# Performance work log

Measured on AMD Instinct MI355X. Metric: run time of the kernel, lower is better.

## Reference

```python
import jax, jax.numpy as jnp
import numpy as np

N_NODES = 50000
N_EDGES = 800000
D_IN = 128
D_HID = 128
N_CLASSES = 16
N_GRAPHS = 256


def _gcn_norm(edge_index, num_nodes):
    # PyG GCNConv default: add self-loops, symmetric normalization.
    loops = jnp.arange(num_nodes, dtype=edge_index.dtype)
    src = jnp.concatenate([edge_index[0], loops])
    dst = jnp.concatenate([edge_index[1], loops])
    deg = jax.ops.segment_sum(jnp.ones_like(src, dtype=jnp.float32), dst,
                              num_segments=num_nodes)
    dinv = jnp.where(deg > 0, jax.lax.rsqrt(deg), 0.0)
    norm = dinv[src] * dinv[dst]  # [E + N]
    return src, dst, norm


def _gcn_conv(x, src, dst, norm, W, b, num_nodes):
    h = x @ W                                  # [N, d_out] dense GEMM
    msg = h[src] * norm[:, None]               # gather + scale [E+N, d_out]
    agg = jax.ops.segment_sum(msg, dst, num_segments=num_nodes)
    return agg + b


def setup_inputs() -> dict:
    key = jax.random.key(0)
    ks = jax.random.split(key, 10)
    x = jax.random.normal(ks[0], (N_NODES, D_IN), dtype=jnp.float32)
    edge_index = jax.random.randint(ks[1], (2, N_EDGES), 0, N_NODES, dtype=jnp.int64)
    batch = jnp.sort(jax.random.randint(ks[2], (N_NODES,), 0, N_GRAPHS, dtype=jnp.int64))
    s1 = 1.0 / np.sqrt(D_IN)
    s2 = 1.0 / np.sqrt(D_HID)
    W1 = jax.random.uniform(ks[3], (D_IN, D_HID), jnp.float32, -s1, s1)
    b1 = jnp.zeros((D_HID,), jnp.float32)
    W2 = jax.random.uniform(ks[4], (D_HID, D_HID), jnp.float32, -s2, s2)
    b2 = jnp.zeros((D_HID,), jnp.float32)
    Wc = jax.random.uniform(ks[5], (D_HID, N_CLASSES), jnp.float32, -s2, s2)
    bc = jnp.zeros((N_CLASSES,), jnp.float32)
    return {"x": x, "edge_index": edge_index, "batch": batch,
            "W1": W1, "b1": b1, "W2": W2, "b2": b2, "Wc": Wc, "bc": bc}


def reference(x, edge_index, batch, W1, b1, W2, b2, Wc, bc):
    src, dst, norm = _gcn_norm(edge_index, N_NODES)
    h = _gcn_conv(x, src, dst, norm, W1, b1, N_NODES)
    h = jax.nn.relu(h)  # dropout is identity in eval mode
    h = _gcn_conv(h, src, dst, norm, W2, b2, N_NODES)
    # global mean pool over graph ids
    sums = jax.ops.segment_sum(h, batch, num_segments=N_GRAPHS)
    cnts = jax.ops.segment_sum(jnp.ones((N_NODES,), jnp.float32), batch,
                               num_segments=N_GRAPHS)
    pooled = sums / jnp.maximum(cnts, 1.0)[:, None]  # [G, D_HID]
    return pooled @ Wc + bc  # [G, N_CLASSES]
```

## Files before the change

### kernel.cpp

```cpp
#include <hip/hip_runtime.h>

#define N_NODES 50000
#define N_EDGES 800000
#define D 128
#define N_GRAPHS 256
#define N_CLASSES 16
#define NB_SCAN ((N_NODES + 255) / 256)

typedef unsigned short ushort_t;
typedef unsigned int uint_t;
typedef unsigned char uchar_t;
typedef __attribute__((ext_vector_type(8))) short bf16x8;
typedef __attribute__((ext_vector_type(4))) float f32x4;
typedef __attribute__((ext_vector_type(4))) int i32x4;

__device__ __forceinline__ float bf2f(uint_t u) {
  return __uint_as_float(u << 16);
}
__device__ __forceinline__ uint_t f2bf(float f) {
  uint_t x = __float_as_uint(f);
  return (x + 0x7fffu + ((x >> 16) & 1u)) >> 16;
}
__device__ __forceinline__ void add8(float* acc, uint4 v) {
  acc[0] += bf2f(v.x & 0xffffu);
  acc[1] += bf2f(v.x >> 16);
  acc[2] += bf2f(v.y & 0xffffu);
  acc[3] += bf2f(v.y >> 16);
  acc[4] += bf2f(v.z & 0xffffu);
  acc[5] += bf2f(v.z >> 16);
  acc[6] += bf2f(v.w & 0xffffu);
  acc[7] += bf2f(v.w >> 16);
}

__global__ void k_pre(const int* __restrict__ ei, int* __restrict__ deg,
                      uchar_t* __restrict__ rank) {
  int e = blockIdx.x * blockDim.x + threadIdx.x;
  if (e < N_EDGES) {
    int d = ei[N_EDGES + e];
    int r = atomicAdd(&deg[d], 1);
    rank[e] = (uchar_t)r;
  }
}

__global__ __launch_bounds__(256) void k_wprep(const float* __restrict__ W1,
                                               const float* __restrict__ W2,
                                               uint4* __restrict__ W1f,
                                               uint4* __restrict__ W2f) {
  int slot = blockIdx.x * 256 + threadIdx.x;
  const float* W = (slot < 2048) ? W1 : W2;
  uint4* Wf = (slot < 2048) ? W1f : W2f;
  int sl = slot & 2047;
  int lane = sl & 63;
  int s = (sl >> 6) & 3;
  int n = sl >> 8;
  int col = n * 16 + (lane & 15);
  int k0 = s * 32 + (lane >> 4) * 8;
  uint4 o;
  o.x = f2bf(W[(size_t)(k0 + 0) * D + col]) | (f2bf(W[(size_t)(k0 + 1) * D + col]) << 16);
  o.y = f2bf(W[(size_t)(k0 + 2) * D + col]) | (f2bf(W[(size_t)(k0 + 3) * D + col]) << 16);
  o.z = f2bf(W[(size_t)(k0 + 4) * D + col]) | (f2bf(W[(size_t)(k0 + 5) * D + col]) << 16);
  o.w = f2bf(W[(size_t)(k0 + 6) * D + col]) | (f2bf(W[(size_t)(k0 + 7) * D + col]) << 16);
  Wf[sl] = o;
}

__global__ __launch_bounds__(256) void k_bsum(const int* __restrict__ deg,
                                              float* __restrict__ dinv,
                                              int* __restrict__ bsum) {
  int t = threadIdx.x;
  int i = blockIdx.x * 256 + t;
  int pd = 0;
  if (i < N_NODES) {
    int d = deg[i];
    dinv[i] = rsqrtf((float)(d + 1));
    pd = (d + 3) & ~3;
  }
#pragma unroll
  for (int o = 1; o < 64; o <<= 1) pd += __shfl_xor(pd, o);
  __shared__ int ws[4];
  if ((t & 63) == 0) ws[t >> 6] = pd;
  __syncthreads();
  if (t == 0) bsum[blockIdx.x] = ws[0] + ws[1] + ws[2] + ws[3];
}

__global__ __launch_bounds__(256) void k_spart(const int* __restrict__ bsum,
                                               const int* __restrict__ batch,
                                               int* __restrict__ bpre,
                                               float* __restrict__ rcnts) {
  int t = threadIdx.x;
  int lane = t & 63, wid = t >> 6;
  int d = (t < NB_SCAN) ? bsum[t] : 0;
  int v = d;
#pragma unroll
  for (int o = 1; o < 64; o <<= 1) {
    int u = __shfl_up(v, o);
    if (lane >= o) v += u;
  }
  __shared__ int ws[4];
  __shared__ int bound[256];
  if (lane == 63) ws[wid] = v;
  {
    int g = t;
    int lo = 0, hi = N_NODES;
    while (lo < hi) {
      int m = (lo + hi) >> 1;
      if (batch[m] < g) lo = m + 1; else hi = m;
    }
    bound[g] = lo;
  }
  __syncthreads();
  int add = 0;
  for (int w = 0; w < wid; ++w) add += ws[w];
  if (t < NB_SCAN) bpre[t] = v - d + add;
  int cnt = ((t == 255) ? N_NODES : bound[t + 1]) - bound[t];
  rcnts[t] = 1.0f / (float)max(cnt, 1);
}

__global__ __launch_bounds__(256) void k_fill(const int* __restrict__ deg,
                                              const int* __restrict__ bpre,
                                              int* __restrict__ offs) {
  int t = threadIdx.x;
  int i = blockIdx.x * 256 + t;
  int pd = (i < N_NODES) ? ((deg[i] + 3) & ~3) : 0;
  int lane = t & 63, wid = t >> 6;
  int v = pd;
#pragma unroll
  for (int o = 1; o < 64; o <<= 1) {
    int u = __shfl_up(v, o);
    if (lane >= o) v += u;
  }
  __shared__ int ws[4];
  if (lane == 63) ws[wid] = v;
  __syncthreads();
  int add = bpre[blockIdx.x];
  for (int w = 0; w < wid; ++w) add += ws[w];
  if (i < N_NODES) offs[i] = v - pd + add;
}

__global__ void k_csr(const int* __restrict__ ei, const int* __restrict__ offs,
                      const uchar_t* __restrict__ rank, int* __restrict__ csr) {
  int e = blockIdx.x * blockDim.x + threadIdx.x;
  if (e >= N_EDGES) return;
  int s = ei[e];
  int d = ei[N_EDGES + e];
  __builtin_nontemporal_store(s, csr + offs[d] + (int)rank[e]);
}

template <typename TIN>
__global__ __launch_bounds__(256) void k_gemm_mfma(const TIN* __restrict__ A,
                                                   const uint4* __restrict__ Wf,
                                                   const float* __restrict__ dinv,
                                                   ushort_t* __restrict__ Out) {
  int t = threadIdx.x;
  int wv = t >> 6, lane = t & 63;
  int row16 = lane & 15, chunk = lane >> 4;
  int row0 = blockIdx.x * 64 + wv * 16;
  int arow = row0 + row16;
  if (arow >= N_NODES) arow = 0;
  bf16x8 afrag[4];
  if constexpr (sizeof(TIN) == 4) {
    const float* Ar = A + (size_t)arow * D + chunk * 8;
#pragma unroll
    for (int s = 0; s < 4; ++s) {
      float4 lo = *(const float4*)(Ar + s * 32);
      float4 hi = *(const float4*)(Ar + s * 32 + 4);
      uint4 u;
      u.x = f2bf(lo.x) | (f2bf(lo.y) << 16);
      u.y = f2bf(lo.z) | (f2bf(lo.w) << 16);
      u.z = f2bf(hi.x) | (f2bf(hi.y) << 16);
      u.w = f2bf(hi.z) | (f2bf(hi.w) << 16);
      afrag[s] = *(bf16x8*)&u;
    }
  } else {
    const ushort_t* Ar = A + (size_t)arow * D + chunk * 8;
#pragma unroll
    for (int s = 0; s < 4; ++s) afrag[s] = *(const bf16x8*)(Ar + s * 32);
  }
  f32x4 acc[8];
#pragma unroll
  for (int n = 0; n < 8; ++n) acc[n] = (f32x4){0.f, 0.f, 0.f, 0.f};
  const bf16x8* Wb = (const bf16x8*)Wf;
#pragma unroll
  for (int n = 0; n < 8; ++n) {
#pragma unroll
    for (int s = 0; s < 4; ++s) {
      bf16x8 b = Wb[(n * 4 + s) * 64 + lane];
      acc[n] = __builtin_amdgcn_mfma_f32_16x16x32_bf16(afrag[s], b, acc[n], 0, 0, 0);
    }
  }
  int crow0 = row0 + chunk * 4;
  float dv[4];
#pragma unroll
  for (int j = 0; j < 4; ++j)
    dv[j] = (crow0 + j < N_NODES) ? dinv[crow0 + j] : 0.f;
#pragma unroll
  for (int n = 0; n < 8; ++n) {
#pragma unroll
    for (int j = 0; j < 4; ++j) {
      int r = crow0 + j;
      if (r < N_NODES)
        Out[(size_t)r * D + n * 16 + row16] = (ushort_t)f2bf(acc[n][j] * dv[j]);
    }
  }
}

__device__ __forceinline__ void agg_core(const ushort_t* __restrict__ h,
                                         const int* __restrict__ csr,
                                         int beg, int end, int grp, int d0,
                                         float* acc) {
  for (int wb = beg; wb < end; wb += 16) {
    int i0 = wb + grp * 4;
    i32x4 s4 = __builtin_nontemporal_load((const i32x4*)(csr + i0));
    bool b0 = i0 < end, b1 = i0 + 1 < end, b2 = i0 + 2 < end, b3 = i0 + 3 < end;
    uint4 v0, v1, v2, v3;
    if (b0) v0 = *(const uint4*)(h + (size_t)s4.x * D + d0);
    if (b1) v1 = *(const uint4*)(h + (size_t)s4.y * D + d0);
    if (b2) v2 = *(const uint4*)(h + (size_t)s4.z * D + d0);
    if (b3) v3 = *(const uint4*)(h + (size_t)s4.w * D + d0);
    if (b0) add8(acc, v0);
    if (b1) add8(acc, v1);
    if (b2) add8(acc, v2);
    if (b3) add8(acc, v3);
  }
}

__global__ __launch_bounds__(256) void k_agg_relu(const ushort_t* __restrict__ h,
                                                  const int* __restrict__ csr,
                                                  const int* __restrict__ offs,
                                                  const int* __restrict__ deg,
                                                  const float* __restrict__ dinv,
                                                  const float* __restrict__ bias,
                                                  ushort_t* __restrict__ obf) {
  int t = threadIdx.x;
  int wv = t >> 6, lane = t & 63;
  int grp = lane >> 4, gl = lane & 15;
  int d0 = gl * 8;
  int node = blockIdx.x * 4 + wv;
  int beg = offs[node], end = beg + deg[node];
  float acc[8] = {0.f, 0.f, 0.f, 0.f, 0.f, 0.f, 0.f, 0.f};
  agg_core(h, csr, beg, end, grp, d0, acc);
#pragma unroll
  for (int m = 16; m <= 32; m <<= 1) {
#pragma unroll
    for (int i = 0; i < 8; ++i) acc[i] += __shfl_xor(acc[i], m);
  }
  if (grp == 0) {
    uint4 v = *(const uint4*)(h + (size_t)node * D + d0);
    add8(acc, v);
    float sc = dinv[node];
    float4 blo = *(const float4*)(bias + d0);
    float4 bhi = *(const float4*)(bias + d0 + 4);
    acc[0] = fmaf(acc[0], sc, blo.x);
    acc[1] = fmaf(acc[1], sc, blo.y);
    acc[2] = fmaf(acc[2], sc, blo.z);
    acc[3] = fmaf(acc[3], sc, blo.w);
    acc[4] = fmaf(acc[4], sc, bhi.x);
    acc[5] = fmaf(acc[5], sc, bhi.y);
    acc[6] = fmaf(acc[6], sc, bhi.z);
    acc[7] = fmaf(acc[7], sc, bhi.w);
#pragma unroll
    for (int i = 0; i < 8; ++i) acc[i] = fmaxf(acc[i], 0.f);
    uint4 o;
    o.x = f2bf(acc[0]) | (f2bf(acc[1]) << 16);
    o.y = f2bf(acc[2]) | (f2bf(acc[3]) << 16);
    o.z = f2bf(acc[4]) | (f2bf(acc[5]) << 16);
    o.w = f2bf(acc[6]) | (f2bf(acc[7]) << 16);
    *(uint4*)(obf + (size_t)node * D + d0) = o;
  }
}

__global__ __launch_bounds__(256) void k_agg_pool(const ushort_t* __restrict__ h,
                                                   const int* __restrict__ csr,
                                                   const int* __restrict__ offs,
                                                   const int* __restrict__ deg,
                                                   const float* __restrict__ dinv,
                                                   const int* __restrict__ batch,
                                                   const float* __restrict__ rcnts,
                                                   float* __restrict__ sums) {
  __shared__ float pool[128];
  int t = threadIdx.x;
  int wv = t >> 6, lane = t & 63;
  int grp = lane >> 4, gl = lane & 15;
  int d0 = gl * 8;
  int node0 = blockIdx.x * 16;
  int g0 = batch[node0];
  if (t < 128) pool[t] = 0.f;
  __syncthreads();
  float pacc[8] = {0.f, 0.f, 0.f, 0.f, 0.f, 0.f, 0.f, 0.f};
  for (int i = 0; i < 4; ++i) {
    int node = node0 + wv * 4 + i;
    int beg = offs[node], end = beg + deg[node];
    float acc[8] = {0.f, 0.f, 0.f, 0.f, 0.f, 0.f, 0.f, 0.f};
    agg_core(h, csr, beg, end, grp, d0, acc);
#pragma unroll
    for (int m = 16; m <= 32; m <<= 1) {
#pragma unroll
      for (int k = 0; k < 8; ++k) acc[k] += __shfl_xor(acc[k], m);
    }
    if (grp == 0) {
      uint4 v = *(const uint4*)(h + (size_t)node * D + d0);
      add8(acc, v);
      int g = batch[node];
      float sc = dinv[node] * rcnts[g];
      if (g == g0) {
#pragma unroll
        for (int k = 0; k < 8; ++k) pacc[k] = fmaf(acc[k], sc, pacc[k]);
      } else {
#pragma unroll
        for (int k = 0; k < 8; ++k)
          atomicAdd(&sums[(size_t)g * D + d0 + k], acc[k] * sc);
      }
    }
  }
  if (grp == 0) {
#pragma unroll
    for (int k = 0; k < 8; ++k) atomicAdd(&pool[d0 + k], pacc[k]);
  }
  __syncthreads();
  if (t < 128) atomicAdd(&sums[(size_t)g0 * D + t], pool[t]);
}

__global__ __launch_bounds__(128) void k_final(const float* __restrict__ sums,
                                               const float* __restrict__ b2,
                                               const float* __restrict__ Wc,
                                               const float* __restrict__ bc,
                                               float* __restrict__ out) {
  __shared__ float p[128];
  int g = blockIdx.x;
  int t = threadIdx.x;
  p[t] = sums[g * D + t] + b2[t];
  __syncthreads();
  if (t < N_CLASSES) {
    float acc = bc[t];
    for (int k = 0; k < D; ++k) acc = fmaf(p[k], Wc[k * N_CLASSES + t], acc);
    out[g * N_CLASSES + t] = acc;
  }
}

extern "C" void kernel_launch(void* const* d_in, const int* in_sizes, int n_in,
                              void* d_out, int out_size, void* d_ws, size_t ws_size,
                              hipStream_t stream) {
  const float* x = (const float*)d_in[0];
  const int* ei = (const int*)d_in[1];
  const int* batch = (const int*)d_in[2];
  const float* W1 = (const float*)d_in[3];
  const float* b1 = (const float*)d_in[4];
  const float* W2 = (const float*)d_in[5];
  const float* b2 = (const float*)d_in[6];
  const float* Wc = (const float*)d_in[7];
  const float* bc = (const float*)d_in[8];
  float* out = (float*)d_out;

  char* ws = (char*)d_ws;
  size_t off = 0;
  auto alloc = [&](size_t bytes) -> void* {
    void* p = (void*)(ws + off);
    off += (bytes + 255) & ~(size_t)255;
    return p;
  };
  int* deg = (int*)alloc((size_t)N_NODES * 4);
  float* sums = (float*)alloc((size_t)N_GRAPHS * D * 4);
  size_t zero_bytes = off;
  int* offs = (int*)alloc((size_t)N_NODES * 4);
  float* dinv = (float*)alloc((size_t)N_NODES * 4);
  float* rcnts = (float*)alloc((size_t)N_GRAPHS * 4);
  int* bsum = (int*)alloc((size_t)NB_SCAN * 4);
  int* bpre = (int*)alloc((size_t)NB_SCAN * 4);
  uchar_t* rank = (uchar_t*)alloc((size_t)N_EDGES);
  uint4* W1f = (uint4*)alloc((size_t)2048 * 16);
  uint4* W2f = (uint4*)alloc((size_t)2048 * 16);
  int* csr = (int*)alloc(((size_t)N_EDGES + 3 * N_NODES + 16) * 4);
  ushort_t* hbuf = (ushort_t*)alloc((size_t)N_NODES * D * 2);
  ushort_t* x2 = (ushort_t*)alloc((size_t)N_NODES * D * 2);

  hipMemsetAsync(ws, 0, zero_bytes, stream);

  k_pre<<<(N_EDGES + 255) / 256, 256, 0, stream>>>(ei, deg, rank);
  k_wprep<<<16, 256, 0, stream>>>(W1, W2, W1f, W2f);
  k_bsum<<<NB_SCAN, 256, 0, stream>>>(deg, dinv, bsum);
  k_spart<<<1, 256, 0, stream>>>(bsum, batch, bpre, rcnts);
  k_fill<<<NB_SCAN, 256, 0, stream>>>(deg, bpre, offs);
  k_csr<<<(N_EDGES + 255) / 256, 256, 0, stream>>>(ei, offs, rank, csr);

  k_gemm_mfma<float><<<(N_NODES + 63) / 64, 256, 0, stream>>>(x, W1f, dinv, hbuf);
  k_agg_relu<<<N_NODES / 4, 256, 0, stream>>>(hbuf, csr, offs, deg, dinv, b1, x2);
  k_gemm_mfma<ushort_t><<<(N_NODES + 63) / 64, 256, 0, stream>>>(x2, W2f, dinv, hbuf);
  k_agg_pool<<<N_NODES / 16, 256, 0, stream>>>(hbuf, csr, offs, deg, dinv, batch, rcnts, sums);

  k_final<<<N_GRAPHS, 128, 0, stream>>>(sums, b2, Wc, bc, out);
}
```

Baseline: 270.6 us.

## Stage GEMM A tiles in swizzled LDS, merge weight prep, widen pool blocks

Three separate changes. The weight-packing kernel is folded into the degree/bsum kernel as extra blocks, saving one launch. The GEMM now loads the 64-row A tile into LDS with coalesced row-contiguous reads and an XOR swizzle, then reads MFMA fragments from LDS, replacing strided per-lane global loads. The pooling aggregation uses 1024-thread blocks with one node per wave and a per-wave shared reduction instead of shared atomics, which raises parallelism but brings larger blocks and a block-wide barrier.

```diff
diff --git a/kernel.cpp b/kernel.cpp
--- a/kernel.cpp
+++ b/kernel.cpp
@@ -42,31 +42,32 @@
   }
 }
 
-__global__ __launch_bounds__(256) void k_wprep(const float* __restrict__ W1,
-                                               const float* __restrict__ W2,
-                                               uint4* __restrict__ W1f,
-                                               uint4* __restrict__ W2f) {
-  int slot = blockIdx.x * 256 + threadIdx.x;
-  const float* W = (slot < 2048) ? W1 : W2;
-  uint4* Wf = (slot < 2048) ? W1f : W2f;
-  int sl = slot & 2047;
-  int lane = sl & 63;
-  int s = (sl >> 6) & 3;
-  int n = sl >> 8;
-  int col = n * 16 + (lane & 15);
-  int k0 = s * 32 + (lane >> 4) * 8;
-  uint4 o;
-  o.x = f2bf(W[(size_t)(k0 + 0) * D + col]) | (f2bf(W[(size_t)(k0 + 1) * D + col]) << 16);
-  o.y = f2bf(W[(size_t)(k0 + 2) * D + col]) | (f2bf(W[(size_t)(k0 + 3) * D + col]) << 16);
-  o.z = f2bf(W[(size_t)(k0 + 4) * D + col]) | (f2bf(W[(size_t)(k0 + 5) * D + col]) << 16);
-  o.w = f2bf(W[(size_t)(k0 + 6) * D + col]) | (f2bf(W[(size_t)(k0 + 7) * D + col]) << 16);
-  Wf[sl] = o;
-}
-
 __global__ __launch_bounds__(256) void k_bsum(const int* __restrict__ deg,
                                               float* __restrict__ dinv,
-                                              int* __restrict__ bsum) {
-  int t = threadIdx.x;
+                                              int* __restrict__ bsum,
+                                              const float* __restrict__ W1,
+                                              const float* __restrict__ W2,
+                                              uint4* __restrict__ W1f,
+                                              uint4* __restrict__ W2f) {
+  int t = threadIdx.x;
+  if (blockIdx.x >= NB_SCAN) {
+    int slot = (blockIdx.x - NB_SCAN) * 256 + t;
+    const float* W = (slot < 2048) ? W1 : W2;
+    uint4* Wf = (slot < 2048) ? W1f : W2f;
+    int sl = slot & 2047;
+    int lane = sl & 63;
+    int s = (sl >> 6) & 3;
+    int n = sl >> 8;
+    int col = n * 16 + (lane & 15);
+    int k0 = s * 32 + (lane >> 4) * 8;
+    uint4 o;
+    o.x = f2bf(W[(size_t)(k0 + 0) * D + col]) | (f2bf(W[(size_t)(k0 + 1) * D + col]) << 16);
+    o.y = f2bf(W[(size_t)(k0 + 2) * D + col]) | (f2bf(W[(size_t)(k0 + 3) * D + col]) << 16);
+    o.z = f2bf(W[(size_t)(k0 + 4) * D + col]) | (f2bf(W[(size_t)(k0 + 5) * D + col]) << 16);
+    o.w = f2bf(W[(size_t)(k0 + 6) * D + col]) | (f2bf(W[(size_t)(k0 + 7) * D + col]) << 16);
+    Wf[sl] = o;
+    return;
+  }
   int i = blockIdx.x * 256 + t;
   int pd = 0;
   if (i < N_NODES) {
@@ -150,30 +151,45 @@
                                                    const uint4* __restrict__ Wf,
                                                    const float* __restrict__ dinv,
                                                    ushort_t* __restrict__ Out) {
-  int t = threadIdx.x;
+  __shared__ uint4 As[1024];
+  int t = threadIdx.x;
+  int row0 = blockIdx.x * 64;
+  if constexpr (sizeof(TIN) == 4) {
+    uint2* As2 = (uint2*)As;
+#pragma unroll
+    for (int i = 0; i < 8; ++i) {
+      int F = t + 256 * i;
+      int r = F >> 5, f = F & 31;
+      int grow = row0 + r;
+      uint2 u = make_uint2(0, 0);
+      if (grow < N_NODES) {
+        float4 v = *(const float4*)(A + (size_t)grow * D + f * 4);
+        u.x = f2bf(v.x) | (f2bf(v.y) << 16);
+        u.y = f2bf(v.z) | (f2bf(v.w) << 16);
+      }
+      int g = f >> 1;
+      As2[(r * 16 + (g ^ (r & 7))) * 2 + (f & 1)] = u;
+    }
+  } else {
+#pragma unroll
+    for (int i = 0; i < 4; ++i) {
+      int G = t + 256 * i;
+      int r = G >> 4, g = G & 15;
+      int grow = row0 + r;
+      uint4 u = make_uint4(0, 0, 0, 0);
+      if (grow < N_NODES) u = *(const uint4*)(A + (size_t)grow * D + g * 8);
+      As[r * 16 + (g ^ (r & 7))] = u;
+    }
+  }
+  __syncthreads();
   int wv = t >> 6, lane = t & 63;
   int row16 = lane & 15, chunk = lane >> 4;
-  int row0 = blockIdx.x * 64 + wv * 16;
-  int arow = row0 + row16;
-  if (arow >= N_NODES) arow = 0;
+  int rl = wv * 16 + row16;
   bf16x8 afrag[4];
-  if constexpr (sizeof(TIN) == 4) {
-    const float* Ar = A + (size_t)arow * D + chunk * 8;
-#pragma unroll
-    for (int s = 0; s < 4; ++s) {
-      float4 lo = *(const float4*)(Ar + s * 32);
-      float4 hi = *(const float4*)(Ar + s * 32 + 4);
-      uint4 u;
-      u.x = f2bf(lo.x) | (f2bf(lo.y) << 16);
-      u.y = f2bf(lo.z) | (f2bf(lo.w) << 16);
-      u.z = f2bf(hi.x) | (f2bf(hi.y) << 16);
-      u.w = f2bf(hi.z) | (f2bf(hi.w) << 16);
-      afrag[s] = *(bf16x8*)&u;
-    }
-  } else {
-    const ushort_t* Ar = A + (size_t)arow * D + chunk * 8;
-#pragma unroll
-    for (int s = 0; s < 4; ++s) afrag[s] = *(const bf16x8*)(Ar + s * 32);
+#pragma unroll
+  for (int s = 0; s < 4; ++s) {
+    int g = s * 4 + chunk;
+    afrag[s] = *(const bf16x8*)&As[rl * 16 + (g ^ (rl & 7))];
   }
   f32x4 acc[8];
 #pragma unroll
@@ -187,7 +203,8 @@
       acc[n] = __builtin_amdgcn_mfma_f32_16x16x32_bf16(afrag[s], b, acc[n], 0, 0, 0);
     }
   }
-  int crow0 = row0 + chunk * 4;
+  int row0w = row0 + wv * 16;
+  int crow0 = row0w + chunk * 4;
   float dv[4];
 #pragma unroll
   for (int j = 0; j < 4; ++j)
@@ -268,7 +285,7 @@
   }
 }
 
-__global__ __launch_bounds__(256) void k_agg_pool(const ushort_t* __restrict__ h,
+__global__ __launch_bounds__(1024) void k_agg_pool(const ushort_t* __restrict__ h,
                                                    const int* __restrict__ csr,
                                                    const int* __restrict__ offs,
                                                    const int* __restrict__ deg,
@@ -276,47 +293,45 @@
                                                    const int* __restrict__ batch,
                                                    const float* __restrict__ rcnts,
                                                    float* __restrict__ sums) {
-  __shared__ float pool[128];
+  __shared__ float pool2[16][128];
   int t = threadIdx.x;
   int wv = t >> 6, lane = t & 63;
   int grp = lane >> 4, gl = lane & 15;
   int d0 = gl * 8;
   int node0 = blockIdx.x * 16;
+  int node = node0 + wv;
   int g0 = batch[node0];
-  if (t < 128) pool[t] = 0.f;
-  __syncthreads();
-  float pacc[8] = {0.f, 0.f, 0.f, 0.f, 0.f, 0.f, 0.f, 0.f};
-  for (int i = 0; i < 4; ++i) {
-    int node = node0 + wv * 4 + i;
-    int beg = offs[node], end = beg + deg[node];
-    float acc[8] = {0.f, 0.f, 0.f, 0.f, 0.f, 0.f, 0.f, 0.f};
-    agg_core(h, csr, beg, end, grp, d0, acc);
-#pragma unroll
-    for (int m = 16; m <= 32; m <<= 1) {
-#pragma unroll
-      for (int k = 0; k < 8; ++k) acc[k] += __shfl_xor(acc[k], m);
-    }
-    if (grp == 0) {
-      uint4 v = *(const uint4*)(h + (size_t)node * D + d0);
-      add8(acc, v);
-      int g = batch[node];
-      float sc = dinv[node] * rcnts[g];
-      if (g == g0) {
-#pragma unroll
-        for (int k = 0; k < 8; ++k) pacc[k] = fmaf(acc[k], sc, pacc[k]);
-      } else {
-#pragma unroll
-        for (int k = 0; k < 8; ++k)
-          atomicAdd(&sums[(size_t)g * D + d0 + k], acc[k] * sc);
+  int beg = offs[node], end = beg + deg[node];
+  float acc[8] = {0.f, 0.f, 0.f, 0.f, 0.f, 0.f, 0.f, 0.f};
+  agg_core(h, csr, beg, end, grp, d0, acc);
+#pragma unroll
+  for (int m = 16; m <= 32; m <<= 1) {
+#pragma unroll
+    for (int k = 0; k < 8; ++k) acc[k] += __shfl_xor(acc[k], m);
+  }
+  if (grp == 0) {
+    uint4 v = *(const uint4*)(h + (size_t)node * D + d0);
+    add8(acc, v);
+    int g = batch[node];
+    float sc = dinv[node] * rcnts[g];
+    if (g == g0) {
+#pragma unroll
+      for (int k = 0; k < 8; ++k) pool2[wv][d0 + k] = acc[k] * sc;
+    } else {
+#pragma unroll
+      for (int k = 0; k < 8; ++k) {
+        pool2[wv][d0 + k] = 0.f;
+        atomicAdd(&sums[(size_t)g * D + d0 + k], acc[k] * sc);
       }
     }
   }
-  if (grp == 0) {
-#pragma unroll
-    for (int k = 0; k < 8; ++k) atomicAdd(&pool[d0 + k], pacc[k]);
-  }
-  __syncthreads();
-  if (t < 128) atomicAdd(&sums[(size_t)g0 * D + t], pool[t]);
+  __syncthreads();
+  if (t < 128) {
+    float s = 0.f;
+#pragma unroll
+    for (int w = 0; w < 16; ++w) s += pool2[w][t];
+    atomicAdd(&sums[(size_t)g0 * D + t], s);
+  }
 }
 
 __global__ __launch_bounds__(128) void k_final(const float* __restrict__ sums,
@@ -375,8 +390,7 @@
   hipMemsetAsync(ws, 0, zero_bytes, stream);
 
   k_pre<<<(N_EDGES + 255) / 256, 256, 0, stream>>>(ei, deg, rank);
-  k_wprep<<<16, 256, 0, stream>>>(W1, W2, W1f, W2f);
-  k_bsum<<<NB_SCAN, 256, 0, stream>>>(deg, dinv, bsum);
+  k_bsum<<<NB_SCAN + 16, 256, 0, stream>>>(deg, dinv, bsum, W1, W2, W1f, W2f);
   k_spart<<<1, 256, 0, stream>>>(bsum, batch, bpre, rcnts);
   k_fill<<<NB_SCAN, 256, 0, stream>>>(deg, bpre, offs);
   k_csr<<<(N_EDGES + 255) / 256, 256, 0, stream>>>(ei, offs, rank, csr);
@@ -384,7 +398,7 @@
   k_gemm_mfma<float><<<(N_NODES + 63) / 64, 256, 0, stream>>>(x, W1f, dinv, hbuf);
   k_agg_relu<<<N_NODES / 4, 256, 0, stream>>>(hbuf, csr, offs, deg, dinv, b1, x2);
   k_gemm_mfma<ushort_t><<<(N_NODES + 63) / 64, 256, 0, stream>>>(x2, W2f, dinv, hbuf);
-  k_agg_pool<<<N_NODES / 16, 256, 0, stream>>>(hbuf, csr, offs, deg, dinv, batch, rcnts, sums);
+  k_agg_pool<<<N_NODES / 16, 1024, 0, stream>>>(hbuf, csr, offs, deg, dinv, batch, rcnts, sums);
 
   k_final<<<N_GRAPHS, 128, 0, stream>>>(sums, b2, Wc, bc, out);
 }
```

Result: no change. 267.7 us (-1.1%).
